# Optimization experiments

Measured on AMD Instinct MI355X. Metric: run time of the kernel, lower is better.

The kernel has to match this reference:

```python
import jax, jax.numpy as jnp
import numpy as np

N = 50000      # nodes
E = 640000     # edges
F_IN = 128     # input features
H = 128        # hidden = 2**7
C = 40         # classes


def setup_inputs() -> dict:
    key = jax.random.key(0)
    ks = jax.random.split(key, 10)
    x = jax.random.normal(ks[0], (N, F_IN), dtype=jnp.float32)
    edge_index = jax.random.randint(ks[1], (2, E), 0, N, dtype=jnp.int32)
    edge_weight = jax.random.uniform(ks[2], (E,), dtype=jnp.float32)
    def glorot(k, fan_in, fan_out):
        s = (6.0 / (fan_in + fan_out)) ** 0.5
        return jax.random.uniform(k, (fan_in, fan_out), jnp.float32, -s, s)
    return {
        "x": x,
        "edge_index": edge_index,
        "edge_weight": edge_weight,
        "W1": glorot(ks[3], F_IN, H), "b1": jnp.zeros((H,), jnp.float32),
        "W2": glorot(ks[4], H, H),    "b2": jnp.zeros((H,), jnp.float32),
        "W3": glorot(ks[5], H, C),    "b3": jnp.zeros((C,), jnp.float32),
    }


def gcn_conv(x, W, b, src, dst, ew, n):
    """PyG GCNConv: add self-loops, symmetric deg normalization, gather-scatter-add."""
    loop = jnp.arange(n, dtype=src.dtype)
    src_sl = jnp.concatenate([src, loop])
    dst_sl = jnp.concatenate([dst, loop])
    w_sl = jnp.concatenate([ew, jnp.ones((n,), ew.dtype)])
    deg = jax.ops.segment_sum(w_sl, dst_sl, num_segments=n)         # [N]
    dinv = jnp.where(deg > 0, jax.lax.rsqrt(deg), 0.0)
    norm = dinv[src_sl] * w_sl * dinv[dst_sl]                        # [E+N]
    h = x @ W                                                        # [N, out]
    msg = h[src_sl] * norm[:, None]                                  # gather + scale
    out = jax.ops.segment_sum(msg, dst_sl, num_segments=n)          # scatter-add
    return out + b


def reference(x, edge_index, edge_weight, W1, b1, W2, b2, W3, b3):
    # eval-mode forward: dropout and dropedge are identity (training=False)
    src, dst = edge_index[0], edge_index[1]
    n = x.shape[0]
    h = jax.nn.relu(gcn_conv(x, W1, b1, src, dst, edge_weight, n))
    h = jax.nn.relu(gcn_conv(h, W2, b2, src, dst, edge_weight, n))
    return gcn_conv(h, W3, b3, src, dst, edge_weight, n)
```

## Files before the change

kernel.cpp:

```cpp
#include <hip/hip_runtime.h>
#include <hip/hip_fp16.h>

constexpr int N_NODES = 50000;
constexpr int N_EDGES = 640000;

constexpr int NBLK  = 256;
constexpr int EPB   = N_EDGES / NBLK;
constexpr int NBUCK = (N_NODES + 255) / 256;
constexpr int GBM   = (N_NODES + 63) / 64;

typedef _Float16 half8  __attribute__((ext_vector_type(8)));
typedef _Float16 half4v __attribute__((ext_vector_type(4)));
typedef float    floatx4 __attribute__((ext_vector_type(4)));


__global__ void wconv_k(const float* __restrict__ W1, const float* __restrict__ W2,
                        const float* __restrict__ W3, _Float16* __restrict__ Wt1,
                        _Float16* __restrict__ Wt2, _Float16* __restrict__ Wt3) {
    int i = blockIdx.x * 256 + threadIdx.x;
    if (i < 16384) {
        int n = i >> 7, k = i & 127;
        Wt1[n * 128 + k] = (_Float16)W1[k * 128 + n];
    } else if (i < 32768) {
        int j = i - 16384; int n = j >> 7, k = j & 127;
        Wt2[n * 128 + k] = (_Float16)W2[k * 128 + n];
    } else if (i < 32768 + 6144) {
        int j = i - 32768; int n = j >> 7, k = j & 127;
        Wt3[n * 128 + k] = (_Float16)((n < 40) ? W3[k * 40 + n] : 0.f);
    }
}


template<typename TIN, int F_OUT, int NT, bool FUSE_HIST>
__global__ __launch_bounds__(256) void gemm_mfma_k(const TIN* __restrict__ X,
        const _Float16* __restrict__ Wt, __half* __restrict__ H,
        const int* __restrict__ dst, int* __restrict__ gh) {
    if constexpr (FUSE_HIST) {
        if (blockIdx.x < NBLK) {
            __shared__ int lh[256];
            int t = threadIdx.x, b = blockIdx.x;
            lh[t] = 0;
            __syncthreads();
            int e0 = b * EPB;
            for (int j = t; j < EPB; j += 256)
                atomicAdd(&lh[dst[e0 + j] >> 8], 1);
            __syncthreads();
            if (t < NBUCK) gh[b * NBUCK + t] = lh[t];
            return;
        }
    }
    int bid = FUSE_HIST ? (int)blockIdx.x - NBLK : (int)blockIdx.x;

    __shared__ _Float16 Xs[64 * 136];
    int tid = threadIdx.x;
    int row0 = bid * 64;

    if constexpr (sizeof(TIN) == 4) {
        for (int idx = tid; idx < 2048; idx += 256) {
            int r = idx >> 5, c4 = idx & 31;
            float4 v = {0.f, 0.f, 0.f, 0.f};
            if (row0 + r < N_NODES)
                v = *(const float4*)((const float*)X + (size_t)(row0 + r) * 128 + c4 * 4);
            half4v h;
            h[0] = (_Float16)v.x; h[1] = (_Float16)v.y;
            h[2] = (_Float16)v.z; h[3] = (_Float16)v.w;
            *(half4v*)&Xs[r * 136 + c4 * 4] = h;
        }
    } else {
        for (int idx = tid; idx < 1024; idx += 256) {
            int r = idx >> 4, c8 = idx & 15;
            int4 v = {0, 0, 0, 0};
            if (row0 + r < N_NODES)
                v = *(const int4*)((const __half*)X + (size_t)(row0 + r) * 128 + c8 * 8);
            *(int4*)&Xs[r * 136 + c8 * 8] = v;
        }
    }
    __syncthreads();

    int lane = tid & 63;
    int wv   = tid >> 6;
    int m    = lane & 15;
    int q    = lane >> 4;

    half8 af[4];
    #pragma unroll
    for (int kt = 0; kt < 4; kt++)
        af[kt] = *(const half8*)&Xs[(wv * 16 + m) * 136 + kt * 32 + q * 8];

    floatx4 acc[NT];
    #pragma unroll
    for (int nt = 0; nt < NT; nt++) { acc[nt][0] = 0.f; acc[nt][1] = 0.f; acc[nt][2] = 0.f; acc[nt][3] = 0.f; }

    #pragma unroll
    for (int nt = 0; nt < NT; nt++) {
        const _Float16* wp = Wt + (size_t)(nt * 16 + m) * 128 + q * 8;
        half8 b0 = *(const half8*)(wp);
        half8 b1 = *(const half8*)(wp + 32);
        half8 b2 = *(const half8*)(wp + 64);
        half8 b3 = *(const half8*)(wp + 96);
        acc[nt] = __builtin_amdgcn_mfma_f32_16x16x32_f16(af[0], b0, acc[nt], 0, 0, 0);
        acc[nt] = __builtin_amdgcn_mfma_f32_16x16x32_f16(af[1], b1, acc[nt], 0, 0, 0);
        acc[nt] = __builtin_amdgcn_mfma_f32_16x16x32_f16(af[2], b2, acc[nt], 0, 0, 0);
        acc[nt] = __builtin_amdgcn_mfma_f32_16x16x32_f16(af[3], b3, acc[nt], 0, 0, 0);
    }

    #pragma unroll
    for (int nt = 0; nt < NT; nt++) {
        #pragma unroll
        for (int r = 0; r < 4; r++)
            Xs[(wv * 16 + q * 4 + r) * 136 + nt * 16 + m] = (_Float16)acc[nt][r];
    }

    if constexpr (F_OUT == 128) {
        for (int g = lane; g < 256; g += 64) {
            int r = g >> 4, c8 = g & 15;
            int row = row0 + wv * 16 + r;
            if (row < N_NODES)
                *(int4*)((__half*)H + (size_t)row * 128 + c8 * 8) =
                    *(const int4*)&Xs[(wv * 16 + r) * 136 + c8 * 8];
        }
    } else {
        for (int g = lane; g < 80; g += 64) {
            int r = g / 5, seg = g - r * 5;
            int row = row0 + wv * 16 + r;
            if (row < N_NODES)
                *(int4*)((__half*)H + (size_t)row * 40 + seg * 8) =
                    *(const int4*)&Xs[(wv * 16 + r) * 136 + seg * 8];
        }
    }
}


__global__ __launch_bounds__(256) void scan1_k(int* __restrict__ gh, int* __restrict__ total) {
    __shared__ int s[256];
    int t = threadIdx.x, b = blockIdx.x;
    int v = gh[t * NBUCK + b];
    s[t] = v;
    __syncthreads();
    int x = v;
    for (int off = 1; off < 256; off <<= 1) {
        int u = (t >= off) ? s[t - off] : 0;
        __syncthreads();
        x += u; s[t] = x;
        __syncthreads();
    }
    gh[t * NBUCK + b] = x - v;
    if (t == 255) total[b] = x;
}

__global__ __launch_bounds__(256) void scan2_k(const int* __restrict__ total,
                                               int* __restrict__ bbase) {
    __shared__ int s[256];
    int t = threadIdx.x;
    int v = (t < NBUCK) ? total[t] : 0;
    s[t] = v;
    __syncthreads();
    int x = v;
    for (int off = 1; off < 256; off <<= 1) {
        int u = (t >= off) ? s[t - off] : 0;
        __syncthreads();
        x += u; s[t] = x;
        __syncthreads();
    }
    if (t <= NBUCK) bbase[t] = x - v;
}


__global__ __launch_bounds__(256) void bucket_k(const int* __restrict__ src,
        const int* __restrict__ dst, const float* __restrict__ ew,
        const int* __restrict__ gh, const int* __restrict__ bbase,
        int2* __restrict__ bkt) {
    __shared__ int cur[256];
    int t = threadIdx.x, b = blockIdx.x;
    if (t < NBUCK) cur[t] = bbase[t] + gh[b * NBUCK + t];
    __syncthreads();
    int e0 = b * EPB;
    for (int j = t; j < EPB; j += 256) {
        int d = dst[e0 + j];
        int pos = atomicAdd(&cur[d >> 8], 1);
        bkt[pos] = make_int2(src[e0 + j] | (d << 16), __float_as_int(ew[e0 + j]));
    }
}


__global__ __launch_bounds__(256) void final_k(const int2* __restrict__ bkt,
        const int* __restrict__ bbase, int2* __restrict__ ev,
        int* __restrict__ rowptr, float* __restrict__ dinv) {
    __shared__ int   cnt[256];
    __shared__ float wsum[256];
    __shared__ int   s[256];
    int t = threadIdx.x, b = blockIdx.x;
    int base = bbase[b], cntb = bbase[b + 1] - base;
    cnt[t] = 0; wsum[t] = 0.f;
    __syncthreads();
    for (int j = t; j < cntb; j += 256) {
        int2 r = bkt[base + j];
        int bin = (r.x >> 16) & 255;
        atomicAdd(&cnt[bin], 1);
        atomicAdd(&wsum[bin], __int_as_float(r.y));
    }
    __syncthreads();
    int v = cnt[t];
    s[t] = v;
    __syncthreads();
    int x = v;
    for (int off = 1; off < 256; off <<= 1) {
        int u = (t >= off) ? s[t - off] : 0;
        __syncthreads();
        x += u; s[t] = x;
        __syncthreads();
    }
    int off_t = x - v;
    int nd = b * 256 + t;
    if (nd < N_NODES) {
        rowptr[nd] = base + off_t;
        dinv[nd] = rsqrtf(1.0f + wsum[t]);
    }
    if (b == 0 && t == 0) rowptr[N_NODES] = N_EDGES;
    s[t] = off_t;
    __syncthreads();
    for (int j = t; j < cntb; j += 256) {
        int2 r = bkt[base + j];
        int bin = (r.x >> 16) & 255;
        int p = atomicAdd(&s[bin], 1);
        ev[base + p] = make_int2(r.x & 0xFFFF, r.y);
    }
}


__global__ __launch_bounds__(256) void agg128_k(const __half* __restrict__ H,
        const int2* __restrict__ ev, const int* __restrict__ rowptr,
        const float* __restrict__ dinv, const float* __restrict__ bias,
        __half* __restrict__ out) {
    int lane = threadIdx.x & 63;
    int node = __builtin_amdgcn_readfirstlane(blockIdx.x * 4 + (threadIdx.x >> 6));
    if (node >= N_NODES) return;
    const __half2* __restrict__ H2 = (const __half2*)H;
    float di = dinv[node];
    float2 hs = __half22float2(H2[(size_t)node * 64 + lane]);
    float ax = di * hs.x, ay = di * hs.y;
    int e0 = rowptr[node], e1 = rowptr[node + 1];
    int e = e0;
    for (; e + 4 <= e1; e += 4) {
        int2 p0 = ev[e + 0];
        int2 p1 = ev[e + 1];
        int2 p2 = ev[e + 2];
        int2 p3 = ev[e + 3];
        float d0 = dinv[p0.x], d1 = dinv[p1.x], d2 = dinv[p2.x], d3 = dinv[p3.x];
        float2 g0 = __half22float2(H2[(size_t)p0.x * 64 + lane]);
        float2 g1 = __half22float2(H2[(size_t)p1.x * 64 + lane]);
        float2 g2 = __half22float2(H2[(size_t)p2.x * 64 + lane]);
        float2 g3 = __half22float2(H2[(size_t)p3.x * 64 + lane]);
        float v0 = __int_as_float(p0.y) * d0;
        float v1 = __int_as_float(p1.y) * d1;
        float v2 = __int_as_float(p2.y) * d2;
        float v3 = __int_as_float(p3.y) * d3;
        ax = fmaf(v0, g0.x, ax); ay = fmaf(v0, g0.y, ay);
        ax = fmaf(v1, g1.x, ax); ay = fmaf(v1, g1.y, ay);
        ax = fmaf(v2, g2.x, ax); ay = fmaf(v2, g2.y, ay);
        ax = fmaf(v3, g3.x, ax); ay = fmaf(v3, g3.y, ay);
    }
    for (; e < e1; e++) {
        int2 p = ev[e];
        float v = __int_as_float(p.y) * dinv[p.x];
        float2 g = __half22float2(H2[(size_t)p.x * 64 + lane]);
        ax = fmaf(v, g.x, ax);
        ay = fmaf(v, g.y, ay);
    }
    float2 b = *(const float2*)&bias[2 * lane];
    ax = fmaxf(fmaf(ax, di, b.x), 0.f);
    ay = fmaxf(fmaf(ay, di, b.y), 0.f);
    ((__half2*)out)[(size_t)node * 64 + lane] = __float22half2_rn(make_float2(ax, ay));
}


__global__ __launch_bounds__(256) void agg40_k(const __half* __restrict__ Y,
        const int2* __restrict__ ev, const int* __restrict__ rowptr,
        const float* __restrict__ dinv, const float* __restrict__ bias,
        float* __restrict__ out) {
    int lane = threadIdx.x & 63;
    int node = __builtin_amdgcn_readfirstlane(blockIdx.x * 4 + (threadIdx.x >> 6));
    if (node >= N_NODES) return;
    const __half2* __restrict__ Y2 = (const __half2*)Y;
    int f = (lane < 20) ? lane : 0;
    float di = dinv[node];
    float2 ys = __half22float2(Y2[(size_t)node * 20 + f]);
    float ax = di * ys.x, ay = di * ys.y;
    int e0 = rowptr[node], e1 = rowptr[node + 1];
    int e = e0;
    for (; e + 4 <= e1; e += 4) {
        int2 p0 = ev[e + 0];
        int2 p1 = ev[e + 1];
        int2 p2 = ev[e + 2];
        int2 p3 = ev[e + 3];
        float d0 = dinv[p0.x], d1 = dinv[p1.x], d2 = dinv[p2.x], d3 = dinv[p3.x];
        float2 g0 = __half22float2(Y2[(size_t)p0.x * 20 + f]);
        float2 g1 = __half22float2(Y2[(size_t)p1.x * 20 + f]);
        float2 g2 = __half22float2(Y2[(size_t)p2.x * 20 + f]);
        float2 g3 = __half22float2(Y2[(size_t)p3.x * 20 + f]);
        float v0 = __int_as_float(p0.y) * d0;
        float v1 = __int_as_float(p1.y) * d1;
        float v2 = __int_as_float(p2.y) * d2;
        float v3 = __int_as_float(p3.y) * d3;
        ax = fmaf(v0, g0.x, ax); ay = fmaf(v0, g0.y, ay);
        ax = fmaf(v1, g1.x, ax); ay = fmaf(v1, g1.y, ay);
        ax = fmaf(v2, g2.x, ax); ay = fmaf(v2, g2.y, ay);
        ax = fmaf(v3, g3.x, ax); ay = fmaf(v3, g3.y, ay);
    }
    for (; e < e1; e++) {
        int2 p = ev[e];
        float v = __int_as_float(p.y) * dinv[p.x];
        float2 g = __half22float2(Y2[(size_t)p.x * 20 + f]);
        ax = fmaf(v, g.x, ax);
        ay = fmaf(v, g.y, ay);
    }
    if (lane < 20) {
        float2 b = *(const float2*)&bias[2 * lane];
        float2 o;
        o.x = fmaf(ax, di, b.x);
        o.y = fmaf(ay, di, b.y);
        *(float2*)&out[(size_t)node * 40 + 2 * lane] = o;
    }
}


extern "C" void kernel_launch(void* const* d_in, const int* in_sizes, int n_in,
                              void* d_out, int out_size, void* d_ws, size_t ws_size,
                              hipStream_t stream) {
    const float* x  = (const float*)d_in[0];
    const int*   ei = (const int*)d_in[1];
    const int*   src = ei;
    const int*   dst = ei + N_EDGES;
    const float* ew = (const float*)d_in[2];
    const float* W1 = (const float*)d_in[3];
    const float* b1 = (const float*)d_in[4];
    const float* W2 = (const float*)d_in[5];
    const float* b2 = (const float*)d_in[6];
    const float* W3 = (const float*)d_in[7];
    const float* b3 = (const float*)d_in[8];
    float* out = (float*)d_out;

    char* w = (char*)d_ws;
    auto alloc = [&](size_t bytes) {
        char* p = w;
        w += (bytes + 255) & ~(size_t)255;
        return p;
    };
    float*     dinv   = (float*)    alloc((size_t)N_NODES * 4);
    int*       rowptr = (int*)      alloc((size_t)(N_NODES + 1) * 4);
    int*       gh     = (int*)      alloc((size_t)NBLK * NBUCK * 4);
    int*       total  = (int*)      alloc((size_t)NBUCK * 4);
    int*       bbase  = (int*)      alloc((size_t)(NBUCK + 1) * 4);
    int2*      bkt    = (int2*)     alloc((size_t)N_EDGES * 8);
    int2*      ev     = (int2*)     alloc((size_t)N_EDGES * 8);
    __half*    hbuf   = (__half*)   alloc((size_t)N_NODES * 128 * 2);
    __half*    abuf   = (__half*)   alloc((size_t)N_NODES * 128 * 2);
    __half*    ybuf   = (__half*)   alloc((size_t)N_NODES * 40 * 2);
    _Float16*  Wt1    = (_Float16*) alloc((size_t)128 * 128 * 2);
    _Float16*  Wt2    = (_Float16*) alloc((size_t)128 * 128 * 2);
    _Float16*  Wt3    = (_Float16*) alloc((size_t)48 * 128 * 2);

    constexpr int GA = (N_NODES + 3) / 4;

    wconv_k<<<152, 256, 0, stream>>>(W1, W2, W3, Wt1, Wt2, Wt3);
    gemm_mfma_k<float, 128, 8, true><<<NBLK + GBM, 256, 0, stream>>>(x, Wt1, hbuf, dst, gh);
    scan1_k<<<NBUCK, 256, 0, stream>>>(gh, total);
    scan2_k<<<1, 256, 0, stream>>>(total, bbase);
    bucket_k<<<NBLK, 256, 0, stream>>>(src, dst, ew, gh, bbase, bkt);
    final_k<<<NBUCK, 256, 0, stream>>>(bkt, bbase, ev, rowptr, dinv);

    agg128_k<<<GA, 256, 0, stream>>>(hbuf, ev, rowptr, dinv, b1, abuf);
    gemm_mfma_k<__half, 128, 8, false><<<GBM, 256, 0, stream>>>(abuf, Wt2, hbuf, nullptr, nullptr);
    agg128_k<<<GA, 256, 0, stream>>>(hbuf, ev, rowptr, dinv, b2, abuf);
    gemm_mfma_k<__half, 40, 3, false><<<GBM, 256, 0, stream>>>(abuf, Wt3, ybuf, nullptr, nullptr);
    agg40_k<<<GA, 256, 0, stream>>>(ybuf, ev, rowptr, dinv, b3, out);
}
```

Before: 251.9 us.

## Precompute packed fp16 edge norms and split feature aggregation into column slices

A new norm_k kernel computes the full symmetric normalization per edge once and packs the 16-bit source index with an fp16 norm into a single int. The aggregation kernels then read 4 bytes per edge instead of 8 and no longer gather dinv[src]. agg128 is also restructured so each block covers a 16-column slice for 16 nodes, with 4 nodes per wavefront, which is meant to improve cache locality of the gathered feature rows. In exchange it adds an extra serial per-node kernel, loses precision by storing the norm in fp16, and relies on node indices fitting in 16 bits.

Measured after the change: 279.1 us. 10.8% more time.

```diff
diff --git a/kernel.cpp b/kernel.cpp
--- a/kernel.cpp
+++ b/kernel.cpp
@@ -228,54 +228,76 @@
 }
 
 
-__global__ __launch_bounds__(256) void agg128_k(const __half* __restrict__ H,
-        const int2* __restrict__ ev, const int* __restrict__ rowptr,
+__global__ void norm_k(const int2* __restrict__ ev, const int* __restrict__ rowptr,
+                       const float* __restrict__ dinv, int* __restrict__ evc) {
+    int i = blockIdx.x * 256 + threadIdx.x;
+    if (i >= N_NODES) return;
+    int e0 = rowptr[i], e1 = rowptr[i + 1];
+    float di = dinv[i];
+    for (int e = e0; e < e1; e++) {
+        int2 p = ev[e];
+        float nrm = __int_as_float(p.y) * dinv[p.x] * di;
+        unsigned short hb = __half_as_ushort(__float2half_rn(nrm));
+        evc[e] = (p.x & 0xFFFF) | ((int)hb << 16);
+    }
+}
+
+
+__global__ __launch_bounds__(256) void agg128s_k(const __half* __restrict__ H,
+        const int* __restrict__ evc, const int* __restrict__ rowptr,
         const float* __restrict__ dinv, const float* __restrict__ bias,
         __half* __restrict__ out) {
-    int lane = threadIdx.x & 63;
-    int node = __builtin_amdgcn_readfirstlane(blockIdx.x * 4 + (threadIdx.x >> 6));
+    int slice = blockIdx.x & 3;
+    int chunk = blockIdx.x >> 2;
+    int tid  = threadIdx.x;
+    int lane = tid & 63;
+    int wv   = tid >> 6;
+    int g    = lane >> 4;
+    int f    = lane & 15;
+    int node = chunk * 16 + wv * 4 + g;
     if (node >= N_NODES) return;
     const __half2* __restrict__ H2 = (const __half2*)H;
+    int col = slice * 16 + f;
     float di = dinv[node];
-    float2 hs = __half22float2(H2[(size_t)node * 64 + lane]);
-    float ax = di * hs.x, ay = di * hs.y;
+    float sn = di * di;
+    float2 hs = __half22float2(H2[(size_t)node * 64 + col]);
+    float ax = sn * hs.x, ay = sn * hs.y;
     int e0 = rowptr[node], e1 = rowptr[node + 1];
     int e = e0;
     for (; e + 4 <= e1; e += 4) {
-        int2 p0 = ev[e + 0];
-        int2 p1 = ev[e + 1];
-        int2 p2 = ev[e + 2];
-        int2 p3 = ev[e + 3];
-        float d0 = dinv[p0.x], d1 = dinv[p1.x], d2 = dinv[p2.x], d3 = dinv[p3.x];
-        float2 g0 = __half22float2(H2[(size_t)p0.x * 64 + lane]);
-        float2 g1 = __half22float2(H2[(size_t)p1.x * 64 + lane]);
-        float2 g2 = __half22float2(H2[(size_t)p2.x * 64 + lane]);
-        float2 g3 = __half22float2(H2[(size_t)p3.x * 64 + lane]);
-        float v0 = __int_as_float(p0.y) * d0;
-        float v1 = __int_as_float(p1.y) * d1;
-        float v2 = __int_as_float(p2.y) * d2;
-        float v3 = __int_as_float(p3.y) * d3;
-        ax = fmaf(v0, g0.x, ax); ay = fmaf(v0, g0.y, ay);
-        ax = fmaf(v1, g1.x, ax); ay = fmaf(v1, g1.y, ay);
-        ax = fmaf(v2, g2.x, ax); ay = fmaf(v2, g2.y, ay);
-        ax = fmaf(v3, g3.x, ax); ay = fmaf(v3, g3.y, ay);
+        int v0 = evc[e + 0];
+        int v1 = evc[e + 1];
+        int v2 = evc[e + 2];
+        int v3 = evc[e + 3];
+        float2 g0 = __half22float2(H2[(size_t)(v0 & 0xFFFF) * 64 + col]);
+        float2 g1 = __half22float2(H2[(size_t)(v1 & 0xFFFF) * 64 + col]);
+        float2 g2 = __half22float2(H2[(size_t)(v2 & 0xFFFF) * 64 + col]);
+        float2 g3 = __half22float2(H2[(size_t)(v3 & 0xFFFF) * 64 + col]);
+        float w0 = __half2float(__ushort_as_half((unsigned short)((unsigned)v0 >> 16)));
+        float w1 = __half2float(__ushort_as_half((unsigned short)((unsigned)v1 >> 16)));
+        float w2 = __half2float(__ushort_as_half((unsigned short)((unsigned)v2 >> 16)));
+        float w3 = __half2float(__ushort_as_half((unsigned short)((unsigned)v3 >> 16)));
+        ax = fmaf(w0, g0.x, ax); ay = fmaf(w0, g0.y, ay);
+        ax = fmaf(w1, g1.x, ax); ay = fmaf(w1, g1.y, ay);
+        ax = fmaf(w2, g2.x, ax); ay = fmaf(w2, g2.y, ay);
+        ax = fmaf(w3, g3.x, ax); ay = fmaf(w3, g3.y, ay);
     }
     for (; e < e1; e++) {
-        int2 p = ev[e];
-        float v = __int_as_float(p.y) * dinv[p.x];
-        float2 g = __half22float2(H2[(size_t)p.x * 64 + lane]);
-        ax = fmaf(v, g.x, ax);
-        ay = fmaf(v, g.y, ay);
-    }
-    float2 b = *(const float2*)&bias[2 * lane];
-    ax = fmaxf(fmaf(ax, di, b.x), 0.f);
-    ay = fmaxf(fmaf(ay, di, b.y), 0.f);
-    ((__half2*)out)[(size_t)node * 64 + lane] = __float22half2_rn(make_float2(ax, ay));
+        int v = evc[e];
+        float2 gv = __half22float2(H2[(size_t)(v & 0xFFFF) * 64 + col]);
+        float w = __half2float(__ushort_as_half((unsigned short)((unsigned)v >> 16)));
+        ax = fmaf(w, gv.x, ax);
+        ay = fmaf(w, gv.y, ay);
+    }
+    float2 b = *(const float2*)&bias[slice * 32 + 2 * f];
+    ax = fmaxf(ax + b.x, 0.f);
+    ay = fmaxf(ay + b.y, 0.f);
+    ((__half2*)out)[(size_t)node * 64 + col] = __float22half2_rn(make_float2(ax, ay));
 }
 
 
 __global__ __launch_bounds__(256) void agg40_k(const __half* __restrict__ Y,
-        const int2* __restrict__ ev, const int* __restrict__ rowptr,
+        const int* __restrict__ evc, const int* __restrict__ rowptr,
         const float* __restrict__ dinv, const float* __restrict__ bias,
         float* __restrict__ out) {
     int lane = threadIdx.x & 63;
@@ -284,41 +306,41 @@
     const __half2* __restrict__ Y2 = (const __half2*)Y;
     int f = (lane < 20) ? lane : 0;
     float di = dinv[node];
+    float sn = di * di;
     float2 ys = __half22float2(Y2[(size_t)node * 20 + f]);
-    float ax = di * ys.x, ay = di * ys.y;
+    float ax = sn * ys.x, ay = sn * ys.y;
     int e0 = rowptr[node], e1 = rowptr[node + 1];
     int e = e0;
     for (; e + 4 <= e1; e += 4) {
-        int2 p0 = ev[e + 0];
-        int2 p1 = ev[e + 1];
-        int2 p2 = ev[e + 2];
-        int2 p3 = ev[e + 3];
-        float d0 = dinv[p0.x], d1 = dinv[p1.x], d2 = dinv[p2.x], d3 = dinv[p3.x];
-        float2 g0 = __half22float2(Y2[(size_t)p0.x * 20 + f]);
-        float2 g1 = __half22float2(Y2[(size_t)p1.x * 20 + f]);
-        float2 g2 = __half22float2(Y2[(size_t)p2.x * 20 + f]);
-        float2 g3 = __half22float2(Y2[(size_t)p3.x * 20 + f]);
-        float v0 = __int_as_float(p0.y) * d0;
-        float v1 = __int_as_float(p1.y) * d1;
-        float v2 = __int_as_float(p2.y) * d2;
-        float v3 = __int_as_float(p3.y) * d3;
-        ax = fmaf(v0, g0.x, ax); ay = fmaf(v0, g0.y, ay);
-        ax = fmaf(v1, g1.x, ax); ay = fmaf(v1, g1.y, ay);
-        ax = fmaf(v2, g2.x, ax); ay = fmaf(v2, g2.y, ay);
-        ax = fmaf(v3, g3.x, ax); ay = fmaf(v3, g3.y, ay);
+        int v0 = evc[e + 0];
+        int v1 = evc[e + 1];
+        int v2 = evc[e + 2];
+        int v3 = evc[e + 3];
+        float2 g0 = __half22float2(Y2[(size_t)(v0 & 0xFFFF) * 20 + f]);
+        float2 g1 = __half22float2(Y2[(size_t)(v1 & 0xFFFF) * 20 + f]);
+        float2 g2 = __half22float2(Y2[(size_t)(v2 & 0xFFFF) * 20 + f]);
+        float2 g3 = __half22float2(Y2[(size_t)(v3 & 0xFFFF) * 20 + f]);
+        float w0 = __half2float(__ushort_as_half((unsigned short)((unsigned)v0 >> 16)));
+        float w1 = __half2float(__ushort_as_half((unsigned short)((unsigned)v1 >> 16)));
+        float w2 = __half2float(__ushort_as_half((unsigned short)((unsigned)v2 >> 16)));
+        float w3 = __half2float(__ushort_as_half((unsigned short)((unsigned)v3 >> 16)));
+        ax = fmaf(w0, g0.x, ax); ay = fmaf(w0, g0.y, ay);
+        ax = fmaf(w1, g1.x, ax); ay = fmaf(w1, g1.y, ay);
+        ax = fmaf(w2, g2.x, ax); ay = fmaf(w2, g2.y, ay);
+        ax = fmaf(w3, g3.x, ax); ay = fmaf(w3, g3.y, ay);
     }
     for (; e < e1; e++) {
-        int2 p = ev[e];
-        float v = __int_as_float(p.y) * dinv[p.x];
-        float2 g = __half22float2(Y2[(size_t)p.x * 20 + f]);
-        ax = fmaf(v, g.x, ax);
-        ay = fmaf(v, g.y, ay);
+        int v = evc[e];
+        float2 gv = __half22float2(Y2[(size_t)(v & 0xFFFF) * 20 + f]);
+        float w = __half2float(__ushort_as_half((unsigned short)((unsigned)v >> 16)));
+        ax = fmaf(w, gv.x, ax);
+        ay = fmaf(w, gv.y, ay);
     }
     if (lane < 20) {
         float2 b = *(const float2*)&bias[2 * lane];
         float2 o;
-        o.x = fmaf(ax, di, b.x);
-        o.y = fmaf(ay, di, b.y);
+        o.x = ax + b.x;
+        o.y = ay + b.y;
         *(float2*)&out[(size_t)node * 40 + 2 * lane] = o;
     }
 }
@@ -353,6 +375,7 @@
     int*       bbase  = (int*)      alloc((size_t)(NBUCK + 1) * 4);
     int2*      bkt    = (int2*)     alloc((size_t)N_EDGES * 8);
     int2*      ev     = (int2*)     alloc((size_t)N_EDGES * 8);
+    int*       evc    = (int*)      alloc((size_t)N_EDGES * 4);
     __half*    hbuf   = (__half*)   alloc((size_t)N_NODES * 128 * 2);
     __half*    abuf   = (__half*)   alloc((size_t)N_NODES * 128 * 2);
     __half*    ybuf   = (__half*)   alloc((size_t)N_NODES * 40 * 2);
@@ -360,7 +383,9 @@
     _Float16*  Wt2    = (_Float16*) alloc((size_t)128 * 128 * 2);
     _Float16*  Wt3    = (_Float16*) alloc((size_t)48 * 128 * 2);
 
-    constexpr int GA = (N_NODES + 3) / 4;
+    int gN = (N_NODES + 255) / 256;
+    constexpr int GA   = (N_NODES + 3) / 4;
+    constexpr int GAS  = ((N_NODES + 15) / 16) * 4;
 
     wconv_k<<<152, 256, 0, stream>>>(W1, W2, W3, Wt1, Wt2, Wt3);
     gemm_mfma_k<float, 128, 8, true><<<NBLK + GBM, 256, 0, stream>>>(x, Wt1, hbuf, dst, gh);
@@ -368,10 +393,11 @@
     scan2_k<<<1, 256, 0, stream>>>(total, bbase);
     bucket_k<<<NBLK, 256, 0, stream>>>(src, dst, ew, gh, bbase, bkt);
     final_k<<<NBUCK, 256, 0, stream>>>(bkt, bbase, ev, rowptr, dinv);
-
-    agg128_k<<<GA, 256, 0, stream>>>(hbuf, ev, rowptr, dinv, b1, abuf);
+    norm_k<<<gN, 256, 0, stream>>>(ev, rowptr, dinv, evc);
+
+    agg128s_k<<<GAS, 256, 0, stream>>>(hbuf, evc, rowptr, dinv, b1, abuf);
     gemm_mfma_k<__half, 128, 8, false><<<GBM, 256, 0, stream>>>(abuf, Wt2, hbuf, nullptr, nullptr);
-    agg128_k<<<GA, 256, 0, stream>>>(hbuf, ev, rowptr, dinv, b2, abuf);
+    agg128s_k<<<GAS, 256, 0, stream>>>(hbuf, evc, rowptr, dinv, b2, abuf);
     gemm_mfma_k<__half, 40, 3, false><<<GBM, 256, 0, stream>>>(abuf, Wt3, ybuf, nullptr, nullptr);
-    agg40_k<<<GA, 256, 0, stream>>>(ybuf, ev, rowptr, dinv, b3, out);
-}
+    agg40_k<<<GA, 256, 0, stream>>>(ybuf, evc, rowptr, dinv, b3, out);
+}
```

## Precompute compact fp16 edge norms in first aggregation and merge scan kernels

Applied to the files above, without the earlier changes.

The first aggregation pass now writes a packed 32-bit edge record holding the 16-bit source index and the fp16 full normalization (w·dinv[src]·dinv[dst]). Later aggregations read these records instead of 8-byte edge entries plus a random dinv gather, and unroll the loop by 8. Separately, scan2 is folded into scan1 through a last-block atomic counter, which saves one launch. The cost is fp16 rounding of edge weights and an extra store stream in the first aggregation.

New measurement: 266.9 us. +6.0%, slower.

```diff
diff --git a/kernel.cpp b/kernel.cpp
--- a/kernel.cpp
+++ b/kernel.cpp
@@ -16,8 +16,10 @@
 
 __global__ void wconv_k(const float* __restrict__ W1, const float* __restrict__ W2,
                         const float* __restrict__ W3, _Float16* __restrict__ Wt1,
-                        _Float16* __restrict__ Wt2, _Float16* __restrict__ Wt3) {
+                        _Float16* __restrict__ Wt2, _Float16* __restrict__ Wt3,
+                        int* __restrict__ flag) {
     int i = blockIdx.x * 256 + threadIdx.x;
+    if (i == 0) *flag = 0;
     if (i < 16384) {
         int n = i >> 7, k = i & 127;
         Wt1[n * 128 + k] = (_Float16)W1[k * 128 + n];
@@ -131,8 +133,10 @@
 }
 
 
-__global__ __launch_bounds__(256) void scan1_k(int* __restrict__ gh, int* __restrict__ total) {
+__global__ __launch_bounds__(256) void scan1_k(int* __restrict__ gh, int* __restrict__ total,
+                                               int* __restrict__ bbase, int* __restrict__ flag) {
     __shared__ int s[256];
+    __shared__ int amLast;
     int t = threadIdx.x, b = blockIdx.x;
     int v = gh[t * NBUCK + b];
     s[t] = v;
@@ -146,23 +150,22 @@
     }
     gh[t * NBUCK + b] = x - v;
     if (t == 255) total[b] = x;
-}
-
-__global__ __launch_bounds__(256) void scan2_k(const int* __restrict__ total,
-                                               int* __restrict__ bbase) {
-    __shared__ int s[256];
-    int t = threadIdx.x;
-    int v = (t < NBUCK) ? total[t] : 0;
-    s[t] = v;
-    __syncthreads();
-    int x = v;
+    __threadfence();
+    if (t == 0) amLast = (atomicAdd(flag, 1) == NBUCK - 1);
+    __syncthreads();
+    if (!amLast) return;
+    __threadfence();
+    int tv = (t < NBUCK) ? total[t] : 0;
+    s[t] = tv;
+    __syncthreads();
+    int tx = tv;
     for (int off = 1; off < 256; off <<= 1) {
         int u = (t >= off) ? s[t - off] : 0;
         __syncthreads();
-        x += u; s[t] = x;
-        __syncthreads();
-    }
-    if (t <= NBUCK) bbase[t] = x - v;
+        tx += u; s[t] = tx;
+        __syncthreads();
+    }
+    if (t <= NBUCK) bbase[t] = tx - tv;
 }
 
 
@@ -228,10 +231,10 @@
 }
 
 
-__global__ __launch_bounds__(256) void agg128_k(const __half* __restrict__ H,
+__global__ __launch_bounds__(256) void agg128_ev_k(const __half* __restrict__ H,
         const int2* __restrict__ ev, const int* __restrict__ rowptr,
         const float* __restrict__ dinv, const float* __restrict__ bias,
-        __half* __restrict__ out) {
+        __half* __restrict__ out, int* __restrict__ evc) {
     int lane = threadIdx.x & 63;
     int node = __builtin_amdgcn_readfirstlane(blockIdx.x * 4 + (threadIdx.x >> 6));
     if (node >= N_NODES) return;
@@ -255,6 +258,12 @@
         float v1 = __int_as_float(p1.y) * d1;
         float v2 = __int_as_float(p2.y) * d2;
         float v3 = __int_as_float(p3.y) * d3;
+        if (lane == 0) {
+            evc[e + 0] = p0.x | ((int)__half_as_ushort(__float2half_rn(v0 * di)) << 16);
+            evc[e + 1] = p1.x | ((int)__half_as_ushort(__float2half_rn(v1 * di)) << 16);
+            evc[e + 2] = p2.x | ((int)__half_as_ushort(__float2half_rn(v2 * di)) << 16);
+            evc[e + 3] = p3.x | ((int)__half_as_ushort(__float2half_rn(v3 * di)) << 16);
+        }
         ax = fmaf(v0, g0.x, ax); ay = fmaf(v0, g0.y, ay);
         ax = fmaf(v1, g1.x, ax); ay = fmaf(v1, g1.y, ay);
         ax = fmaf(v2, g2.x, ax); ay = fmaf(v2, g2.y, ay);
@@ -264,6 +273,8 @@
         int2 p = ev[e];
         float v = __int_as_float(p.y) * dinv[p.x];
         float2 g = __half22float2(H2[(size_t)p.x * 64 + lane]);
+        if (lane == 0)
+            evc[e] = p.x | ((int)__half_as_ushort(__float2half_rn(v * di)) << 16);
         ax = fmaf(v, g.x, ax);
         ay = fmaf(v, g.y, ay);
     }
@@ -274,8 +285,51 @@
 }
 
 
+__global__ __launch_bounds__(256) void agg128_evc_k(const __half* __restrict__ H,
+        const int* __restrict__ evc, const int* __restrict__ rowptr,
+        const float* __restrict__ dinv, const float* __restrict__ bias,
+        __half* __restrict__ out) {
+    int lane = threadIdx.x & 63;
+    int node = __builtin_amdgcn_readfirstlane(blockIdx.x * 4 + (threadIdx.x >> 6));
+    if (node >= N_NODES) return;
+    const __half2* __restrict__ H2 = (const __half2*)H;
+    float di = dinv[node];
+    float sn = di * di;
+    float2 hs = __half22float2(H2[(size_t)node * 64 + lane]);
+    float ax = sn * hs.x, ay = sn * hs.y;
+    int e0 = rowptr[node], e1 = rowptr[node + 1];
+    int e = e0;
+    for (; e + 8 <= e1; e += 8) {
+        int v[8];
+        #pragma unroll
+        for (int j = 0; j < 8; j++) v[j] = evc[e + j];
+        float2 g[8];
+        #pragma unroll
+        for (int j = 0; j < 8; j++)
+            g[j] = __half22float2(H2[(size_t)(v[j] & 0xFFFF) * 64 + lane]);
+        #pragma unroll
+        for (int j = 0; j < 8; j++) {
+            float w = __half2float(__ushort_as_half((unsigned short)((unsigned)v[j] >> 16)));
+            ax = fmaf(w, g[j].x, ax);
+            ay = fmaf(w, g[j].y, ay);
+        }
+    }
+    for (; e < e1; e++) {
+        int v = evc[e];
+        float2 gv = __half22float2(H2[(size_t)(v & 0xFFFF) * 64 + lane]);
+        float w = __half2float(__ushort_as_half((unsigned short)((unsigned)v >> 16)));
+        ax = fmaf(w, gv.x, ax);
+        ay = fmaf(w, gv.y, ay);
+    }
+    float2 b = *(const float2*)&bias[2 * lane];
+    ax = fmaxf(ax + b.x, 0.f);
+    ay = fmaxf(ay + b.y, 0.f);
+    ((__half2*)out)[(size_t)node * 64 + lane] = __float22half2_rn(make_float2(ax, ay));
+}
+
+
 __global__ __launch_bounds__(256) void agg40_k(const __half* __restrict__ Y,
-        const int2* __restrict__ ev, const int* __restrict__ rowptr,
+        const int* __restrict__ evc, const int* __restrict__ rowptr,
         const float* __restrict__ dinv, const float* __restrict__ bias,
         float* __restrict__ out) {
     int lane = threadIdx.x & 63;
@@ -284,41 +338,38 @@
     const __half2* __restrict__ Y2 = (const __half2*)Y;
     int f = (lane < 20) ? lane : 0;
     float di = dinv[node];
+    float sn = di * di;
     float2 ys = __half22float2(Y2[(size_t)node * 20 + f]);
-    float ax = di * ys.x, ay = di * ys.y;
+    float ax = sn * ys.x, ay = sn * ys.y;
     int e0 = rowptr[node], e1 = rowptr[node + 1];
     int e = e0;
-    for (; e + 4 <= e1; e += 4) {
-        int2 p0 = ev[e + 0];
-        int2 p1 = ev[e + 1];
-        int2 p2 = ev[e + 2];
-        int2 p3 = ev[e + 3];
-        float d0 = dinv[p0.x], d1 = dinv[p1.x], d2 = dinv[p2.x], d3 = dinv[p3.x];
-        float2 g0 = __half22float2(Y2[(size_t)p0.x * 20 + f]);
-        float2 g1 = __half22float2(Y2[(size_t)p1.x * 20 + f]);
-        float2 g2 = __half22float2(Y2[(size_t)p2.x * 20 + f]);
-        float2 g3 = __half22float2(Y2[(size_t)p3.x * 20 + f]);
-        float v0 = __int_as_float(p0.y) * d0;
-        float v1 = __int_as_float(p1.y) * d1;
-        float v2 = __int_as_float(p2.y) * d2;
-        float v3 = __int_as_float(p3.y) * d3;
-        ax = fmaf(v0, g0.x, ax); ay = fmaf(v0, g0.y, ay);
-        ax = fmaf(v1, g1.x, ax); ay = fmaf(v1, g1.y, ay);
-        ax = fmaf(v2, g2.x, ax); ay = fmaf(v2, g2.y, ay);
-        ax = fmaf(v3, g3.x, ax); ay = fmaf(v3, g3.y, ay);
+    for (; e + 8 <= e1; e += 8) {
+        int v[8];
+        #pragma unroll
+        for (int j = 0; j < 8; j++) v[j] = evc[e + j];
+        float2 g[8];
+        #pragma unroll
+        for (int j = 0; j < 8; j++)
+            g[j] = __half22float2(Y2[(size_t)(v[j] & 0xFFFF) * 20 + f]);
+        #pragma unroll
+        for (int j = 0; j < 8; j++) {
+            float w = __half2float(__ushort_as_half((unsigned short)((unsigned)v[j] >> 16)));
+            ax = fmaf(w, g[j].x, ax);
+            ay = fmaf(w, g[j].y, ay);
+        }
     }
     for (; e < e1; e++) {
-        int2 p = ev[e];
-        float v = __int_as_float(p.y) * dinv[p.x];
-        float2 g = __half22float2(Y2[(size_t)p.x * 20 + f]);
-        ax = fmaf(v, g.x, ax);
-        ay = fmaf(v, g.y, ay);
+        int v = evc[e];
+        float2 gv = __half22float2(Y2[(size_t)(v & 0xFFFF) * 20 + f]);
+        float w = __half2float(__ushort_as_half((unsigned short)((unsigned)v >> 16)));
+        ax = fmaf(w, gv.x, ax);
+        ay = fmaf(w, gv.y, ay);
     }
     if (lane < 20) {
         float2 b = *(const float2*)&bias[2 * lane];
         float2 o;
-        o.x = fmaf(ax, di, b.x);
-        o.y = fmaf(ay, di, b.y);
+        o.x = ax + b.x;
+        o.y = ay + b.y;
         *(float2*)&out[(size_t)node * 40 + 2 * lane] = o;
     }
 }
@@ -351,8 +402,10 @@
     int*       gh     = (int*)      alloc((size_t)NBLK * NBUCK * 4);
     int*       total  = (int*)      alloc((size_t)NBUCK * 4);
     int*       bbase  = (int*)      alloc((size_t)(NBUCK + 1) * 4);
+    int*       flag   = (int*)      alloc(256);
     int2*      bkt    = (int2*)     alloc((size_t)N_EDGES * 8);
     int2*      ev     = (int2*)     alloc((size_t)N_EDGES * 8);
+    int*       evc    = (int*)      alloc((size_t)N_EDGES * 4);
     __half*    hbuf   = (__half*)   alloc((size_t)N_NODES * 128 * 2);
     __half*    abuf   = (__half*)   alloc((size_t)N_NODES * 128 * 2);
     __half*    ybuf   = (__half*)   alloc((size_t)N_NODES * 40 * 2);
@@ -362,16 +415,15 @@
 
     constexpr int GA = (N_NODES + 3) / 4;
 
-    wconv_k<<<152, 256, 0, stream>>>(W1, W2, W3, Wt1, Wt2, Wt3);
+    wconv_k<<<152, 256, 0, stream>>>(W1, W2, W3, Wt1, Wt2, Wt3, flag);
     gemm_mfma_k<float, 128, 8, true><<<NBLK + GBM, 256, 0, stream>>>(x, Wt1, hbuf, dst, gh);
-    scan1_k<<<NBUCK, 256, 0, stream>>>(gh, total);
-    scan2_k<<<1, 256, 0, stream>>>(total, bbase);
+    scan1_k<<<NBUCK, 256, 0, stream>>>(gh, total, bbase, flag);
     bucket_k<<<NBLK, 256, 0, stream>>>(src, dst, ew, gh, bbase, bkt);
     final_k<<<NBUCK, 256, 0, stream>>>(bkt, bbase, ev, rowptr, dinv);
 
-    agg128_k<<<GA, 256, 0, stream>>>(hbuf, ev, rowptr, dinv, b1, abuf);
+    agg128_ev_k<<<GA, 256, 0, stream>>>(hbuf, ev, rowptr, dinv, b1, abuf, evc);
     gemm_mfma_k<__half, 128, 8, false><<<GBM, 256, 0, stream>>>(abuf, Wt2, hbuf, nullptr, nullptr);
-    agg128_k<<<GA, 256, 0, stream>>>(hbuf, ev, rowptr, dinv, b2, abuf);
+    agg128_evc_k<<<GA, 256, 0, stream>>>(hbuf, evc, rowptr, dinv, b2, abuf);
     gemm_mfma_k<__half, 40, 3, false><<<GBM, 256, 0, stream>>>(abuf, Wt3, ybuf, nullptr, nullptr);
-    agg40_k<<<GA, 256, 0, stream>>>(ybuf, ev, rowptr, dinv, b3, out);
-}
+    agg40_k<<<GA, 256, 0, stream>>>(ybuf, evc, rowptr, dinv, b3, out);
+}
```
